# Kernel optimization log

Measured on AMD Instinct MI355X. Metric: run time of the kernel, lower is better.

The kernel has to match this reference:

```python
import jax, jax.numpy as jnp
import numpy as np

HIDDEN = 512
NHEADS = 8
ALPHA = 0.1
NUM_HOP = 4
MASK_VAL = -16384.0
LN_EPS = 1e-5


def setup_inputs() -> dict:
    key = jax.random.key(0)
    ks = jax.random.split(key, 10)
    B, N, H = 8, 1024, HIDDEN
    s = 1.0 / np.sqrt(H)
    x = jax.random.normal(ks[0], (B, N, H), dtype=jnp.float32)
    adj = jax.random.randint(ks[1], (B, N, N), 0, 2, dtype=jnp.int32)
    Wq = jax.random.uniform(ks[2], (H, H), jnp.float32, -s, s)
    bq = jax.random.uniform(ks[3], (H,), jnp.float32, -s, s)
    Wk = jax.random.uniform(ks[4], (H, H), jnp.float32, -s, s)
    bk = jax.random.uniform(ks[5], (H,), jnp.float32, -s, s)
    Wv = jax.random.uniform(ks[6], (H, H), jnp.float32, -s, s)
    bv = jax.random.uniform(ks[7], (H,), jnp.float32, -s, s)
    gamma = jnp.ones((H,), jnp.float32)
    beta = jnp.zeros((H,), jnp.float32)
    return {"x": x, "adj": adj, "Wq": Wq, "bq": bq, "Wk": Wk, "bk": bk,
            "Wv": Wv, "bv": bv, "gamma": gamma, "beta": beta}


def reference(x, adj, Wq, bq, Wk, bk, Wv, bv, gamma, beta):
    B, N, H = x.shape
    u = H // NHEADS
    # torch Linear: y = x @ W^T + b
    q = x @ Wq.T + bq  # [B,N,H]
    k = x @ Wk.T + bk
    v = x @ Wv.T + bv
    # split hidden into contiguous head chunks (matches per-head slicing)
    qh = q.reshape(B, N, NHEADS, u).transpose(0, 2, 1, 3)  # [B,Hd,N,u]
    kh = k.reshape(B, N, NHEADS, u).transpose(0, 2, 1, 3)
    vh = v.reshape(B, N, NHEADS, u).transpose(0, 2, 1, 3)
    scores = jnp.einsum('bhnd,bhmd->bhnm', qh, kh)  # [B,Hd,N,N]
    mask = (adj == 0)[:, None, :, :]  # broadcast over heads
    scores = jnp.where(mask, MASK_VAL, scores)
    pros = jax.nn.softmax(scores, axis=-1)
    z_init = vh
    z = z_init
    for _ in range(NUM_HOP):
        z = (1.0 - ALPHA) * jnp.einsum('bhnm,bhmd->bhnd', pros, z) + ALPHA * z_init
    h_prime = z.transpose(0, 2, 1, 3).reshape(B, N, H)  # concat heads
    y = x + h_prime
    mu = jnp.mean(y, axis=-1, keepdims=True)
    var = jnp.mean((y - mu) ** 2, axis=-1, keepdims=True)
    return (y - mu) / jnp.sqrt(var + LN_EPS) * gamma + beta
```

## Files before the change

### kernel.cpp

```cpp
#include <hip/hip_runtime.h>
#include <hip/hip_bf16.h>

#define BB 8
#define NN 1024
#define HH 512
#define NHEADS 8
#define UU 64

typedef __attribute__((ext_vector_type(8))) short short8;
typedef __attribute__((ext_vector_type(4))) float f32x4;
typedef __attribute__((ext_vector_type(16))) float f32x16;
typedef unsigned short u16;
typedef unsigned char u8;

__device__ inline float b2f(unsigned short u) {
    union { float f; unsigned int i; } c; c.i = ((unsigned int)u) << 16; return c.f;
}
__device__ inline unsigned short f2b(float f) {
    __hip_bfloat16 h = __float2bfloat16(f);
    return *reinterpret_cast<unsigned short*>(&h);
}
__device__ inline unsigned int pkbf(float a, float b) {
    unsigned int r;
    asm("v_cvt_pk_bf16_f32 %0, %1, %2" : "=v"(r) : "v"(a), "v"(b));
    return r;
}
__device__ inline float upk_lo(unsigned int u) {
    union { float f; unsigned int i; } c; c.i = u << 16; return c.f;
}
__device__ inline float upk_hi(unsigned int u) {
    union { float f; unsigned int i; } c; c.i = u & 0xffff0000u; return c.f;
}
__device__ inline void gl_lds16(const void* g, void* l) {
    __builtin_amdgcn_global_load_lds(
        (const __attribute__((address_space(1))) unsigned int*)g,
        (__attribute__((address_space(3))) unsigned int*)l, 16, 0, 0);
}

__global__ __launch_bounds__(256) void cvt_all(
    const float* __restrict__ x, const float* __restrict__ Wq,
    const float* __restrict__ Wk, const float* __restrict__ Wv,
    u16* __restrict__ xb, u16* __restrict__ Wb)
{
    const int gid = blockIdx.x;
    const float* src;
    u16* dst;
    int base;
    if (gid < 2048) {
        src = x; dst = xb;
        base = (gid * 256 + threadIdx.x) * 8;
    } else {
        const int g = gid - 2048;
        const int which = g >> 7;
        const int slice = g & 127;
        src = which == 0 ? Wq : (which == 1 ? Wk : Wv);
        dst = Wb + (size_t)which * HH * HH;
        base = (slice * 256 + threadIdx.x) * 8;
    }
    const float4* sp = (const float4*)&src[base];
    float4 a = sp[0], b = sp[1];
    short8 o;
    o[0] = (short)f2b(a.x); o[1] = (short)f2b(a.y);
    o[2] = (short)f2b(a.z); o[3] = (short)f2b(a.w);
    o[4] = (short)f2b(b.x); o[5] = (short)f2b(b.y);
    o[6] = (short)f2b(b.z); o[7] = (short)f2b(b.w);
    *(short8*)&dst[base] = o;
}

__global__ __launch_bounds__(256) void adj_pack(
    const int* __restrict__ adj, unsigned int* __restrict__ adjpT)
{
    const int wave = threadIdx.x >> 6, lane = threadIdx.x & 63;
    const int row = blockIdx.x * 4 + wave;
    const int b = row >> 10, r = row & 1023;
    const int* ar = adj + (size_t)row * NN;
    unsigned int* ob = adjpT + (((size_t)b) << 15) + r;
    #pragma unroll
    for (int it = 0; it < 16; ++it) {
        int a = ar[it * 64 + lane];
        unsigned long long m = __ballot(a != 0);
        if (lane == 0) {
            ob[(size_t)(2 * it)     << 10] = (unsigned int)m;
            ob[(size_t)(2 * it + 1) << 10] = (unsigned int)(m >> 32);
        }
    }
}

__global__ __launch_bounds__(256, 4) void qkv_gemm(
    const u16* __restrict__ xb, const u16* __restrict__ Wb,
    const float* __restrict__ bq, const float* __restrict__ bk,
    const float* __restrict__ bv,
    u16* __restrict__ q, u16* __restrict__ k, u16* __restrict__ v)
{
    const int which = blockIdx.z;
    const u16* W      = Wb + (size_t)which * HH * HH;
    const float* bias = which == 0 ? bq : (which == 1 ? bk : bv);
    u16* out          = which == 0 ? q  : (which == 1 ? k  : v);

    const int tid = threadIdx.x;
    const int wave = tid >> 6, lane = tid & 63;
    const int ln = lane & 15, quad = lane >> 4;
    const int wr = (wave >> 1) * 64, wc = (wave & 1) * 64;
    const int rowbase = blockIdx.x * 128, colbase = blockIdx.y * 128;

    __shared__ __align__(16) char smem[128 * 136 * 2];
    u16* Cs = (u16*)smem;

    f32x4 acc[4][4];
    #pragma unroll
    for (int ri = 0; ri < 4; ++ri)
        #pragma unroll
        for (int ci = 0; ci < 4; ++ci) acc[ri][ci] = (f32x4){0.f, 0.f, 0.f, 0.f};

    const int lr = lane >> 2;
    const int sg = lane & 3;

    auto STAGE = [&](int buf, int kk) {
        char* Ab = smem + buf * 16384;
        char* Bb = smem + 8192 + buf * 16384;
        #pragma unroll
        for (int i = 0; i < 2; ++i) {
            int r = wave * 32 + i * 16 + lr;
            gl_lds16(&xb[(size_t)(rowbase + r) * HH + kk + sg * 8],
                     Ab + (wave * 32 + i * 16) * 64);
            gl_lds16(&W[(size_t)(colbase + r) * HH + kk + sg * 8],
                     Bb + (wave * 32 + i * 16) * 64);
        }
    };

    STAGE(0, 0);
    for (int s = 0; s < 16; ++s) {
        __syncthreads();
        if (s < 15) STAGE((s + 1) & 1, (s + 1) * 32);
        const u16* As = (const u16*)(smem + (s & 1) * 16384);
        const u16* Bs = (const u16*)(smem + 8192 + (s & 1) * 16384);

        short8 bfr[4];
        #pragma unroll
        for (int ci = 0; ci < 4; ++ci)
            bfr[ci] = *(const short8*)&Bs[(wc + ci * 16 + ln) * 32 + quad * 8];
        #pragma unroll
        for (int ri = 0; ri < 4; ++ri) {
            short8 af = *(const short8*)&As[(wr + ri * 16 + ln) * 32 + quad * 8];
            #pragma unroll
            for (int ci = 0; ci < 4; ++ci)
                acc[ri][ci] = __builtin_amdgcn_mfma_f32_16x16x32_bf16(af, bfr[ci], acc[ri][ci], 0, 0, 0);
        }
    }

    __syncthreads();
    #pragma unroll
    for (int ci = 0; ci < 4; ++ci) {
        int col = wc + ci * 16 + ln;
        float bb = bias[colbase + col];
        #pragma unroll
        for (int ri = 0; ri < 4; ++ri) {
            #pragma unroll
            for (int r = 0; r < 4; ++r) {
                int row = wr + ri * 16 + quad * 4 + r;
                Cs[row * 136 + col] = f2b(acc[ri][ci][r] + bb);
            }
        }
    }
    __syncthreads();
    {
        int row = tid >> 1, half = tid & 1;
        int gcol0 = colbase + half * 64;
        int hh = gcol0 >> 6;
        int grow = rowbase + row;
        int bidx = grow >> 10, n = grow & 1023;
        u16* op = &out[(((size_t)(bidx * NHEADS + hh)) * NN + n) * UU];
        const u16* cp = &Cs[row * 136 + half * 64];
        #pragma unroll
        for (int j = 0; j < 8; ++j)
            *(short8*)(op + j * 8) = *(const short8*)(cp + j * 8);
    }
}

__global__ __launch_bounds__(256) void vt8(
    const u16* __restrict__ v, u8* __restrict__ v8t)
{
    const int bh = blockIdx.x >> 4, chunk = blockIdx.x & 15;
    const int t = threadIdx.x;
    const size_t hd = (size_t)bh << 16;
    __shared__ u16 tile[64][72];

    const int n0 = chunk * 64;
    const int r = t >> 2, cs = t & 3;
    const u16* vp = &v[((size_t)bh * NN + n0 + r) * UU + cs * 16];
    short8 a = *(const short8*)vp;
    short8 b8 = *(const short8*)(vp + 8);
    #pragma unroll
    for (int j = 0; j < 8; ++j) {
        tile[r][cs * 16 + j] = (u16)a[j];
        tile[r][cs * 16 + 8 + j] = (u16)b8[j];
    }
    __syncthreads();
    const int c = t & 63, qt = t >> 6;
    unsigned int w[4];
    #pragma unroll
    for (int g = 0; g < 4; ++g) {
        float f0 = b2f(tile[qt * 16 + g * 4 + 0][c]);
        float f1 = b2f(tile[qt * 16 + g * 4 + 1][c]);
        float f2 = b2f(tile[qt * 16 + g * 4 + 2][c]);
        float f3 = b2f(tile[qt * 16 + g * 4 + 3][c]);
        int lo = __builtin_amdgcn_cvt_pk_fp8_f32(f0, f1, 0, false);
        w[g] = (unsigned int)__builtin_amdgcn_cvt_pk_fp8_f32(f2, f3, lo, true);
    }
    uint4 o; o.x = w[0]; o.y = w[1]; o.z = w[2]; o.w = w[3];
    *(uint4*)&v8t[hd + (size_t)c * 1024 + n0 + qt * 16] = o;
}

__device__ inline f32x16 score_tile(const u16* kp, const short8* qf)
{
    short8 kf[4];
    #pragma unroll
    for (int f = 0; f < 4; ++f) kf[f] = *(const short8*)(kp + f * 16);
    f32x16 acc;
    #pragma unroll
    for (int j = 0; j < 16; ++j) acc[j] = 0.f;
    #pragma unroll
    for (int f = 0; f < 4; ++f)
        acc = __builtin_amdgcn_mfma_f32_32x32x16_bf16(kf[f], qf[f], acc, 0, 0, 0);
    return acc;
}

__global__ __launch_bounds__(512, 4) void scores_softmax(
    const u16* __restrict__ q, const u16* __restrict__ kmat,
    const unsigned int* __restrict__ adjpT, u8* __restrict__ P8)
{
    const int gid = blockIdx.x;
    const int j = gid >> 3;
    const int h = gid & 7;
    const int b = j >> 5;
    const int bx = j & 31;
    const int bh = b * NHEADS + h;

    const int tid = threadIdx.x;
    const int kq = tid >> 6, lane = tid & 63;
    const int l31 = lane & 31, hi = lane >> 5;
    const int n = bx * 32 + l31;
    const int kt0 = kq * 4;

    __shared__ float rs[8][32];

    short8 qf[4];
    const u16* qp = &q[((size_t)bh * NN + n) * UU + hi * 8];
    #pragma unroll
    for (int f = 0; f < 4; ++f) qf[f] = *(const short8*)(qp + f * 16);

    const u16* kbase = kmat + (size_t)bh * NN * UU + (size_t)(kt0 * 32 + l31) * UU + hi * 8;
    const unsigned int* mbase = adjpT + (((size_t)b) << 15) + n;

    unsigned int mv[4];
    #pragma unroll
    for (int i = 0; i < 4; ++i)
        mv[i] = mbase[(size_t)(kt0 + i) << 10] >> (4 * hi);

    const float L2E = 1.442695041f;
    const float C0 = -46.16624f;
    const float CM = -100000.0f;

    unsigned int eb[4][4][2];
    float rs0 = 0.f, rs1 = 0.f, rs2 = 0.f, rs3 = 0.f;
    #pragma unroll
    for (int i = 0; i < 4; ++i) {
        f32x16 acc = score_tile(kbase + (size_t)i * (32 * UU), qf);
        const unsigned int m2 = mv[i];
        #pragma unroll
        for (int g = 0; g < 4; ++g) {
            float e[4];
            #pragma unroll
            for (int r = 0; r < 4; ++r) {
                const int koff = r + 8 * g;
                float addv = ((m2 >> koff) & 1u) ? C0 : CM;
                e[r] = __builtin_amdgcn_exp2f(fmaf(L2E, acc[g * 4 + r], addv));
            }
            if (g == 0) rs0 += (e[0] + e[1]) + (e[2] + e[3]);
            else if (g == 1) rs1 += (e[0] + e[1]) + (e[2] + e[3]);
            else if (g == 2) rs2 += (e[0] + e[1]) + (e[2] + e[3]);
            else rs3 += (e[0] + e[1]) + (e[2] + e[3]);
            eb[i][g][0] = pkbf(e[0], e[1]);
            eb[i][g][1] = pkbf(e[2], e[3]);
        }
    }
    float rsum = (rs0 + rs1) + (rs2 + rs3);
    rsum += __shfl_xor(rsum, 32);
    if (lane < 32) rs[kq][lane] = rsum;
    __syncthreads();
    const float total = ((rs[0][l31] + rs[1][l31]) + (rs[2][l31] + rs[3][l31]))
                      + ((rs[4][l31] + rs[5][l31]) + (rs[6][l31] + rs[7][l31]));
    const float scl = 16.0f / total;

    u8* pb = P8 + (((size_t)bh) << 20) + (size_t)(n >> 4) * 16384
           + (n & 15) * 32 + hi * 16;
    #pragma unroll
    for (int i = 0; i < 4; ++i) {
        unsigned int dw[4];
        #pragma unroll
        for (int g = 0; g < 4; ++g) {
            float e0 = upk_lo(eb[i][g][0]) * scl;
            float e1 = upk_hi(eb[i][g][0]) * scl;
            float e2 = upk_lo(eb[i][g][1]) * scl;
            float e3 = upk_hi(eb[i][g][1]) * scl;
            int lo = __builtin_amdgcn_cvt_pk_fp8_f32(e0, e1, 0, false);
            dw[g] = (unsigned int)__builtin_amdgcn_cvt_pk_fp8_f32(e2, e3, lo, true);
        }
        unsigned int sendA = hi ? dw[0] : dw[2];
        unsigned int sendB = hi ? dw[1] : dw[3];
        unsigned int recvA = (unsigned int)__shfl_xor((int)sendA, 32);
        unsigned int recvB = (unsigned int)__shfl_xor((int)sendB, 32);
        uint4 o;
        o.x = hi ? recvA : dw[0];
        o.y = hi ? dw[2] : recvA;
        o.z = hi ? recvB : dw[1];
        o.w = hi ? dw[3] : recvB;
        *(uint4*)(pb + (size_t)(kt0 + i) * 512) = o;
    }
}

__global__ __launch_bounds__(512) void hop(
    const u8* __restrict__ P8, const u8* __restrict__ z8in,
    const u16* __restrict__ v, u8* __restrict__ z8out,
    u16* __restrict__ zbf_out, int last)
{
    const int b = blockIdx.z, h = blockIdx.y, rt = blockIdx.x;
    const int bh = b * NHEADS + h;
    const int tid = threadIdx.x;
    const int wave = tid >> 6, lane = tid & 63;
    const int ln = lane & 15, quad = lane >> 4;
    const int wrow = rt * 128 + wave * 16;

    __shared__ __align__(16) u8 zt[64 * 1040];

    const u8* zg = z8in + ((size_t)bh << 16);
    #pragma unroll
    for (int i = 0; i < 8; ++i) {
        int c = wave * 8 + i;
        gl_lds16(zg + (size_t)c * 1024 + lane * 16, (char*)zt + c * 1040);
    }

    const u8* pt = P8 + ((size_t)bh << 20) + (size_t)(rt * 8 + wave) * 16384
                 + ln * 32 + quad * 8;
    long pa[4];
    #pragma unroll
    for (int i = 0; i < 4; ++i) pa[i] = *(const long*)(pt + i * 512);

    __syncthreads();

    f32x4 acc[4];
    #pragma unroll
    for (int ci = 0; ci < 4; ++ci) acc[ci] = (f32x4){0.f, 0.f, 0.f, 0.f};

    #pragma unroll
    for (int kc = 0; kc < 32; ++kc) {
        long a = pa[kc & 3];
        if (kc + 4 < 32) pa[kc & 3] = *(const long*)(pt + (kc + 4) * 512);
        int kk = kc * 32;
        #pragma unroll
        for (int ci = 0; ci < 4; ++ci) {
            long bz = *(const long*)&zt[(ci * 16 + ln) * 1040 + kk + quad * 8];
            acc[ci] = __builtin_amdgcn_mfma_f32_16x16x32_fp8_fp8(a, bz, acc[ci], 0, 0, 0);
        }
    }

    if (last) {
        #pragma unroll
        for (int ci = 0; ci < 4; ++ci) {
            int col = ci * 16 + ln;
            #pragma unroll
            for (int r = 0; r < 4; ++r) {
                int row = wrow + quad * 4 + r;
                float vv = b2f(v[((size_t)bh * NN + row) * UU + col]);
                zbf_out[((size_t)(b * NN + row)) * HH + h * UU + col]
                    = f2b(0.05625f * acc[ci][r] + 0.1f * vv);
            }
        }
    } else {
        u8* zo = z8out + ((size_t)bh << 16);
        #pragma unroll
        for (int ci = 0; ci < 4; ++ci) {
            int col = ci * 16 + ln;
            float zv[4];
            #pragma unroll
            for (int r = 0; r < 4; ++r) {
                int row = wrow + quad * 4 + r;
                float vv = b2f(v[((size_t)bh * NN + row) * UU + col]);
                zv[r] = 0.05625f * acc[ci][r] + 0.1f * vv;
            }
            int lo = __builtin_amdgcn_cvt_pk_fp8_f32(zv[0], zv[1], 0, false);
            unsigned int dw = (unsigned int)__builtin_amdgcn_cvt_pk_fp8_f32(zv[2], zv[3], lo, true);
            *(unsigned int*)&zo[(size_t)col * 1024 + wrow + quad * 4] = dw;
        }
    }
}

__global__ __launch_bounds__(256) void resid_ln(
    const float* __restrict__ x, const u16* __restrict__ z,
    const float* __restrict__ gamma, const float* __restrict__ beta,
    float* __restrict__ out)
{
    const int r = blockIdx.x * 4 + (threadIdx.x >> 6);
    const int lane = threadIdx.x & 63;
    const size_t base = (size_t)r * HH + lane * 8;

    const float4* xp = (const float4*)&x[base];
    float4 x0 = xp[0], x1 = xp[1];
    short8 zv = *(const short8*)&z[base];
    float y[8];
    y[0] = x0.x + b2f((u16)zv[0]); y[1] = x0.y + b2f((u16)zv[1]);
    y[2] = x0.z + b2f((u16)zv[2]); y[3] = x0.w + b2f((u16)zv[3]);
    y[4] = x1.x + b2f((u16)zv[4]); y[5] = x1.y + b2f((u16)zv[5]);
    y[6] = x1.z + b2f((u16)zv[6]); y[7] = x1.w + b2f((u16)zv[7]);

    float s = 0.f, sq = 0.f;
    #pragma unroll
    for (int j = 0; j < 8; ++j) { s += y[j]; sq += y[j] * y[j]; }
    #pragma unroll
    for (int off = 32; off >= 1; off >>= 1) {
        s  += __shfl_xor(s, off);
        sq += __shfl_xor(sq, off);
    }
    const float mu = s * (1.0f / HH);
    const float var = sq * (1.0f / HH) - mu * mu;
    const float rstd = rsqrtf(var + 1e-5f);

    const float4* gp = (const float4*)&gamma[lane * 8];
    const float4* bp = (const float4*)&beta[lane * 8];
    float4 g0 = gp[0], g1 = gp[1], b0 = bp[0], b1 = bp[1];

    float4 o0, o1;
    o0.x = (y[0] - mu) * rstd * g0.x + b0.x;
    o0.y = (y[1] - mu) * rstd * g0.y + b0.y;
    o0.z = (y[2] - mu) * rstd * g0.z + b0.z;
    o0.w = (y[3] - mu) * rstd * g0.w + b0.w;
    o1.x = (y[4] - mu) * rstd * g1.x + b1.x;
    o1.y = (y[5] - mu) * rstd * g1.y + b1.y;
    o1.z = (y[6] - mu) * rstd * g1.z + b1.z;
    o1.w = (y[7] - mu) * rstd * g1.w + b1.w;
    float4* op = (float4*)&out[base];
    op[0] = o0; op[1] = o1;
}

extern "C" void kernel_launch(void* const* d_in, const int* in_sizes, int n_in,
                              void* d_out, int out_size, void* d_ws, size_t ws_size,
                              hipStream_t stream)
{
    const float* x   = (const float*)d_in[0];
    const int* adj   = (const int*)d_in[1];
    const float* Wq  = (const float*)d_in[2];
    const float* bq  = (const float*)d_in[3];
    const float* Wk  = (const float*)d_in[4];
    const float* bk  = (const float*)d_in[5];
    const float* Wv  = (const float*)d_in[6];
    const float* bv  = (const float*)d_in[7];
    const float* gamma = (const float*)d_in[8];
    const float* beta  = (const float*)d_in[9];
    float* out = (float*)d_out;

    const size_t E = (size_t)BB * NN * HH;
    u16* ws16 = (u16*)d_ws;
    u16* xb = ws16;
    u16* q  = ws16 + E;
    u16* k  = ws16 + 2 * E;
    u16* v  = ws16 + 3 * E;
    u16* za = ws16 + 4 * E;
    u16* Wb = ws16 + 5 * E;
    u8* base8 = (u8*)(ws16 + 5 * E + 786432);
    u8* P8  = base8;
    u8* z8a = base8 + ((size_t)64 << 20);
    u8* z8b = z8a + ((size_t)4 << 20);
    u8* v8t = z8b + ((size_t)4 << 20);
    unsigned int* adjpT = (unsigned int*)(v8t + ((size_t)4 << 20));

    cvt_all<<<dim3(2432), 256, 0, stream>>>(x, Wq, Wk, Wv, xb, Wb);
    adj_pack<<<dim3(2048), 256, 0, stream>>>(adj, adjpT);
    qkv_gemm<<<dim3(64, 4, 3), 256, 0, stream>>>(xb, Wb, bq, bk, bv, q, k, v);
    vt8<<<dim3(1024), 256, 0, stream>>>(v, v8t);
    scores_softmax<<<dim3(2048), 512, 0, stream>>>(q, k, adjpT, P8);
    hop<<<dim3(8, NHEADS, BB), 512, 0, stream>>>(P8, v8t, v, z8a, za, 0);
    hop<<<dim3(8, NHEADS, BB), 512, 0, stream>>>(P8, z8a, v, z8b, za, 0);
    hop<<<dim3(8, NHEADS, BB), 512, 0, stream>>>(P8, z8b, v, z8a, za, 0);
    hop<<<dim3(8, NHEADS, BB), 512, 0, stream>>>(P8, z8a, v, z8b, za, 1);
    resid_ln<<<dim3(2048), 256, 0, stream>>>(x, za, gamma, beta, out);
}
```

Measured before the change: 265.0 us.

## Fuse prep kernels and load hop z operand directly from global

Merges the bf16 conversion and adjacency bit-packing kernels into one launch, saving one kernel launch. The hop kernel no longer stages z into LDS with a block barrier. It instead double-buffers z fragments in registers from global/L2. Its grid is flattened to 1D with head as the fastest index and launch bounds raised for occupancy. This trades LDS reuse across waves for redundant global reads of z, relying on L2 to serve them.

```diff
diff --git a/kernel.cpp b/kernel.cpp
--- a/kernel.cpp
+++ b/kernel.cpp
@@ -37,51 +37,51 @@
         (__attribute__((address_space(3))) unsigned int*)l, 16, 0, 0);
 }
 
-__global__ __launch_bounds__(256) void cvt_all(
+__global__ __launch_bounds__(256) void prep(
     const float* __restrict__ x, const float* __restrict__ Wq,
     const float* __restrict__ Wk, const float* __restrict__ Wv,
-    u16* __restrict__ xb, u16* __restrict__ Wb)
+    const int* __restrict__ adj,
+    u16* __restrict__ xb, u16* __restrict__ Wb,
+    unsigned int* __restrict__ adjpT)
 {
     const int gid = blockIdx.x;
-    const float* src;
-    u16* dst;
-    int base;
-    if (gid < 2048) {
-        src = x; dst = xb;
-        base = (gid * 256 + threadIdx.x) * 8;
+    if (gid < 2432) {
+        const float* src;
+        u16* dst;
+        int base;
+        if (gid < 2048) {
+            src = x; dst = xb;
+            base = (gid * 256 + threadIdx.x) * 8;
+        } else {
+            const int g = gid - 2048;
+            const int which = g >> 7;
+            const int slice = g & 127;
+            src = which == 0 ? Wq : (which == 1 ? Wk : Wv);
+            dst = Wb + (size_t)which * HH * HH;
+            base = (slice * 256 + threadIdx.x) * 8;
+        }
+        const float4* sp = (const float4*)&src[base];
+        float4 a = sp[0], b = sp[1];
+        short8 o;
+        o[0] = (short)f2b(a.x); o[1] = (short)f2b(a.y);
+        o[2] = (short)f2b(a.z); o[3] = (short)f2b(a.w);
+        o[4] = (short)f2b(b.x); o[5] = (short)f2b(b.y);
+        o[6] = (short)f2b(b.z); o[7] = (short)f2b(b.w);
+        *(short8*)&dst[base] = o;
     } else {
-        const int g = gid - 2048;
-        const int which = g >> 7;
-        const int slice = g & 127;
-        src = which == 0 ? Wq : (which == 1 ? Wk : Wv);
-        dst = Wb + (size_t)which * HH * HH;
-        base = (slice * 256 + threadIdx.x) * 8;
-    }
-    const float4* sp = (const float4*)&src[base];
-    float4 a = sp[0], b = sp[1];
-    short8 o;
-    o[0] = (short)f2b(a.x); o[1] = (short)f2b(a.y);
-    o[2] = (short)f2b(a.z); o[3] = (short)f2b(a.w);
-    o[4] = (short)f2b(b.x); o[5] = (short)f2b(b.y);
-    o[6] = (short)f2b(b.z); o[7] = (short)f2b(b.w);
-    *(short8*)&dst[base] = o;
-}
-
-__global__ __launch_bounds__(256) void adj_pack(
-    const int* __restrict__ adj, unsigned int* __restrict__ adjpT)
-{
-    const int wave = threadIdx.x >> 6, lane = threadIdx.x & 63;
-    const int row = blockIdx.x * 4 + wave;
-    const int b = row >> 10, r = row & 1023;
-    const int* ar = adj + (size_t)row * NN;
-    unsigned int* ob = adjpT + (((size_t)b) << 15) + r;
-    #pragma unroll
-    for (int it = 0; it < 16; ++it) {
-        int a = ar[it * 64 + lane];
-        unsigned long long m = __ballot(a != 0);
-        if (lane == 0) {
-            ob[(size_t)(2 * it)     << 10] = (unsigned int)m;
-            ob[(size_t)(2 * it + 1) << 10] = (unsigned int)(m >> 32);
+        const int wave = threadIdx.x >> 6, lane = threadIdx.x & 63;
+        const int row = (gid - 2432) * 4 + wave;
+        const int b = row >> 10, r = row & 1023;
+        const int* ar = adj + (size_t)row * NN;
+        unsigned int* ob = adjpT + (((size_t)b) << 15) + r;
+        #pragma unroll
+        for (int it = 0; it < 16; ++it) {
+            int a = ar[it * 64 + lane];
+            unsigned long long m = __ballot(a != 0);
+            if (lane == 0) {
+                ob[(size_t)(2 * it)     << 10] = (unsigned int)m;
+                ob[(size_t)(2 * it + 1) << 10] = (unsigned int)(m >> 32);
+            }
         }
     }
 }
@@ -319,34 +319,35 @@
     }
 }
 
-__global__ __launch_bounds__(512) void hop(
+__global__ __launch_bounds__(512, 4) void hop(
     const u8* __restrict__ P8, const u8* __restrict__ z8in,
     const u16* __restrict__ v, u8* __restrict__ z8out,
     u16* __restrict__ zbf_out, int last)
 {
-    const int b = blockIdx.z, h = blockIdx.y, rt = blockIdx.x;
+    const int gid = blockIdx.x;
+    const int h = gid & 7;
+    const int j = gid >> 3;
+    const int b = j >> 3;
+    const int rt = j & 7;
     const int bh = b * NHEADS + h;
+
     const int tid = threadIdx.x;
     const int wave = tid >> 6, lane = tid & 63;
     const int ln = lane & 15, quad = lane >> 4;
     const int wrow = rt * 128 + wave * 16;
 
-    __shared__ __align__(16) u8 zt[64 * 1040];
-
-    const u8* zg = z8in + ((size_t)bh << 16);
-    #pragma unroll
-    for (int i = 0; i < 8; ++i) {
-        int c = wave * 8 + i;
-        gl_lds16(zg + (size_t)c * 1024 + lane * 16, (char*)zt + c * 1040);
-    }
-
+    const u8* zg = z8in + ((size_t)bh << 16) + (size_t)ln * 1024 + quad * 8;
     const u8* pt = P8 + ((size_t)bh << 20) + (size_t)(rt * 8 + wave) * 16384
                  + ln * 32 + quad * 8;
+
     long pa[4];
     #pragma unroll
     for (int i = 0; i < 4; ++i) pa[i] = *(const long*)(pt + i * 512);
 
-    __syncthreads();
+    long zb0[4], zb1[4];
+    #pragma unroll
+    for (int ci = 0; ci < 4; ++ci)
+        zb0[ci] = *(const long*)(zg + (size_t)ci * 16384);
 
     f32x4 acc[4];
     #pragma unroll
@@ -354,12 +355,23 @@
 
     #pragma unroll
     for (int kc = 0; kc < 32; ++kc) {
+        if (kc + 1 < 32) {
+            const int kk = (kc + 1) * 32;
+            if (kc & 1) {
+                #pragma unroll
+                for (int ci = 0; ci < 4; ++ci)
+                    zb0[ci] = *(const long*)(zg + (size_t)ci * 16384 + kk);
+            } else {
+                #pragma unroll
+                for (int ci = 0; ci < 4; ++ci)
+                    zb1[ci] = *(const long*)(zg + (size_t)ci * 16384 + kk);
+            }
+        }
         long a = pa[kc & 3];
         if (kc + 4 < 32) pa[kc & 3] = *(const long*)(pt + (kc + 4) * 512);
-        int kk = kc * 32;
         #pragma unroll
         for (int ci = 0; ci < 4; ++ci) {
-            long bz = *(const long*)&zt[(ci * 16 + ln) * 1040 + kk + quad * 8];
+            long bz = (kc & 1) ? zb1[ci] : zb0[ci];
             acc[ci] = __builtin_amdgcn_mfma_f32_16x16x32_fp8_fp8(a, bz, acc[ci], 0, 0, 0);
         }
     }
@@ -473,14 +485,13 @@
     u8* v8t = z8b + ((size_t)4 << 20);
     unsigned int* adjpT = (unsigned int*)(v8t + ((size_t)4 << 20));
 
-    cvt_all<<<dim3(2432), 256, 0, stream>>>(x, Wq, Wk, Wv, xb, Wb);
-    adj_pack<<<dim3(2048), 256, 0, stream>>>(adj, adjpT);
+    prep<<<dim3(4480), 256, 0, stream>>>(x, Wq, Wk, Wv, adj, xb, Wb, adjpT);
     qkv_gemm<<<dim3(64, 4, 3), 256, 0, stream>>>(xb, Wb, bq, bk, bv, q, k, v);
     vt8<<<dim3(1024), 256, 0, stream>>>(v, v8t);
     scores_softmax<<<dim3(2048), 512, 0, stream>>>(q, k, adjpT, P8);
-    hop<<<dim3(8, NHEADS, BB), 512, 0, stream>>>(P8, v8t, v, z8a, za, 0);
-    hop<<<dim3(8, NHEADS, BB), 512, 0, stream>>>(P8, z8a, v, z8b, za, 0);
-    hop<<<dim3(8, NHEADS, BB), 512, 0, stream>>>(P8, z8b, v, z8a, za, 0);
-    hop<<<dim3(8, NHEADS, BB), 512, 0, stream>>>(P8, z8a, v, z8b, za, 1);
+    hop<<<dim3(512), 512, 0, stream>>>(P8, v8t, v, z8a, za, 0);
+    hop<<<dim3(512), 512, 0, stream>>>(P8, z8a, v, z8b, za, 0);
+    hop<<<dim3(512), 512, 0, stream>>>(P8, z8b, v, z8a, za, 0);
+    hop<<<dim3(512), 512, 0, stream>>>(P8, z8a, v, z8b, za, 1);
     resid_ln<<<dim3(2048), 256, 0, stream>>>(x, za, gamma, beta, out);
 }
```

Result: slower. 443.4 us (+67.3%).

## Merge conversion and adjacency-packing kernels; halve hop LDS with two-phase staging

Applied to the files above, without the earlier changes.

The bf16 conversion and adjacency bit-packing kernels are merged into one launch so that one kernel boundary goes away. The hop kernel now stages the z tile into LDS in two 512-column halves, which halves its shared-memory footprint. It also declares launch bounds of four blocks per CU, aiming for higher occupancy. The cost is an extra pair of barriers mid-loop, and the second half's staging is not overlapped with compute. The row-pair interleaved LDS layout also changes the bank access pattern.

```diff
diff --git a/kernel.cpp b/kernel.cpp
--- a/kernel.cpp
+++ b/kernel.cpp
@@ -37,51 +37,51 @@
         (__attribute__((address_space(3))) unsigned int*)l, 16, 0, 0);
 }
 
-__global__ __launch_bounds__(256) void cvt_all(
+__global__ __launch_bounds__(256) void prep(
     const float* __restrict__ x, const float* __restrict__ Wq,
     const float* __restrict__ Wk, const float* __restrict__ Wv,
-    u16* __restrict__ xb, u16* __restrict__ Wb)
+    const int* __restrict__ adj,
+    u16* __restrict__ xb, u16* __restrict__ Wb,
+    unsigned int* __restrict__ adjpT)
 {
     const int gid = blockIdx.x;
-    const float* src;
-    u16* dst;
-    int base;
-    if (gid < 2048) {
-        src = x; dst = xb;
-        base = (gid * 256 + threadIdx.x) * 8;
+    if (gid < 2432) {
+        const float* src;
+        u16* dst;
+        int base;
+        if (gid < 2048) {
+            src = x; dst = xb;
+            base = (gid * 256 + threadIdx.x) * 8;
+        } else {
+            const int g = gid - 2048;
+            const int which = g >> 7;
+            const int slice = g & 127;
+            src = which == 0 ? Wq : (which == 1 ? Wk : Wv);
+            dst = Wb + (size_t)which * HH * HH;
+            base = (slice * 256 + threadIdx.x) * 8;
+        }
+        const float4* sp = (const float4*)&src[base];
+        float4 a = sp[0], b = sp[1];
+        short8 o;
+        o[0] = (short)f2b(a.x); o[1] = (short)f2b(a.y);
+        o[2] = (short)f2b(a.z); o[3] = (short)f2b(a.w);
+        o[4] = (short)f2b(b.x); o[5] = (short)f2b(b.y);
+        o[6] = (short)f2b(b.z); o[7] = (short)f2b(b.w);
+        *(short8*)&dst[base] = o;
     } else {
-        const int g = gid - 2048;
-        const int which = g >> 7;
-        const int slice = g & 127;
-        src = which == 0 ? Wq : (which == 1 ? Wk : Wv);
-        dst = Wb + (size_t)which * HH * HH;
-        base = (slice * 256 + threadIdx.x) * 8;
-    }
-    const float4* sp = (const float4*)&src[base];
-    float4 a = sp[0], b = sp[1];
-    short8 o;
-    o[0] = (short)f2b(a.x); o[1] = (short)f2b(a.y);
-    o[2] = (short)f2b(a.z); o[3] = (short)f2b(a.w);
-    o[4] = (short)f2b(b.x); o[5] = (short)f2b(b.y);
-    o[6] = (short)f2b(b.z); o[7] = (short)f2b(b.w);
-    *(short8*)&dst[base] = o;
-}
-
-__global__ __launch_bounds__(256) void adj_pack(
-    const int* __restrict__ adj, unsigned int* __restrict__ adjpT)
-{
-    const int wave = threadIdx.x >> 6, lane = threadIdx.x & 63;
-    const int row = blockIdx.x * 4 + wave;
-    const int b = row >> 10, r = row & 1023;
-    const int* ar = adj + (size_t)row * NN;
-    unsigned int* ob = adjpT + (((size_t)b) << 15) + r;
-    #pragma unroll
-    for (int it = 0; it < 16; ++it) {
-        int a = ar[it * 64 + lane];
-        unsigned long long m = __ballot(a != 0);
-        if (lane == 0) {
-            ob[(size_t)(2 * it)     << 10] = (unsigned int)m;
-            ob[(size_t)(2 * it + 1) << 10] = (unsigned int)(m >> 32);
+        const int wave = threadIdx.x >> 6, lane = threadIdx.x & 63;
+        const int row = (gid - 2432) * 4 + wave;
+        const int b = row >> 10, r = row & 1023;
+        const int* ar = adj + (size_t)row * NN;
+        unsigned int* ob = adjpT + (((size_t)b) << 15) + r;
+        #pragma unroll
+        for (int it = 0; it < 16; ++it) {
+            int a = ar[it * 64 + lane];
+            unsigned long long m = __ballot(a != 0);
+            if (lane == 0) {
+                ob[(size_t)(2 * it)     << 10] = (unsigned int)m;
+                ob[(size_t)(2 * it + 1) << 10] = (unsigned int)(m >> 32);
+            }
         }
     }
 }
@@ -319,7 +319,7 @@
     }
 }
 
-__global__ __launch_bounds__(512) void hop(
+__global__ __launch_bounds__(512, 4) void hop(
     const u8* __restrict__ P8, const u8* __restrict__ z8in,
     const u16* __restrict__ v, u8* __restrict__ z8out,
     u16* __restrict__ zbf_out, int last)
@@ -331,17 +331,23 @@
     const int ln = lane & 15, quad = lane >> 4;
     const int wrow = rt * 128 + wave * 16;
 
-    __shared__ __align__(16) u8 zt[64 * 1040];
+    __shared__ __align__(16) u8 zt[32 * 1040];
 
     const u8* zg = z8in + ((size_t)bh << 16);
-    #pragma unroll
-    for (int i = 0; i < 8; ++i) {
-        int c = wave * 8 + i;
-        gl_lds16(zg + (size_t)c * 1024 + lane * 16, (char*)zt + c * 1040);
-    }
+    auto STAGEZ = [&](int m0) {
+        #pragma unroll
+        for (int jj = 0; jj < 4; ++jj) {
+            int g = jj * 8 + wave;
+            const u8* src = zg + (size_t)(2 * g + (lane >> 5)) * 1024 + m0
+                          + (lane & 31) * 16;
+            gl_lds16(src, (char*)zt + g * 1040);
+        }
+    };
 
     const u8* pt = P8 + ((size_t)bh << 20) + (size_t)(rt * 8 + wave) * 16384
                  + ln * 32 + quad * 8;
+
+    STAGEZ(0);
     long pa[4];
     #pragma unroll
     for (int i = 0; i < 4; ++i) pa[i] = *(const long*)(pt + i * 512);
@@ -353,13 +359,31 @@
     for (int ci = 0; ci < 4; ++ci) acc[ci] = (f32x4){0.f, 0.f, 0.f, 0.f};
 
     #pragma unroll
-    for (int kc = 0; kc < 32; ++kc) {
+    for (int kc = 0; kc < 16; ++kc) {
+        long a = pa[kc & 3];
+        pa[kc & 3] = *(const long*)(pt + (kc + 4) * 512);
+        int kkl = kc * 32;
+        #pragma unroll
+        for (int ci = 0; ci < 4; ++ci) {
+            int row = ci * 16 + ln;
+            long bz = *(const long*)&zt[(row >> 1) * 1040 + (row & 1) * 512 + kkl + quad * 8];
+            acc[ci] = __builtin_amdgcn_mfma_f32_16x16x32_fp8_fp8(a, bz, acc[ci], 0, 0, 0);
+        }
+    }
+
+    __syncthreads();
+    STAGEZ(512);
+    __syncthreads();
+
+    #pragma unroll
+    for (int kc = 16; kc < 32; ++kc) {
         long a = pa[kc & 3];
         if (kc + 4 < 32) pa[kc & 3] = *(const long*)(pt + (kc + 4) * 512);
-        int kk = kc * 32;
+        int kkl = kc * 32 - 512;
         #pragma unroll
         for (int ci = 0; ci < 4; ++ci) {
-            long bz = *(const long*)&zt[(ci * 16 + ln) * 1040 + kk + quad * 8];
+            int row = ci * 16 + ln;
+            long bz = *(const long*)&zt[(row >> 1) * 1040 + (row & 1) * 512 + kkl + quad * 8];
             acc[ci] = __builtin_amdgcn_mfma_f32_16x16x32_fp8_fp8(a, bz, acc[ci], 0, 0, 0);
         }
     }
@@ -473,8 +497,7 @@
     u8* v8t = z8b + ((size_t)4 << 20);
     unsigned int* adjpT = (unsigned int*)(v8t + ((size_t)4 << 20));
 
-    cvt_all<<<dim3(2432), 256, 0, stream>>>(x, Wq, Wk, Wv, xb, Wb);
-    adj_pack<<<dim3(2048), 256, 0, stream>>>(adj, adjpT);
+    prep<<<dim3(4480), 256, 0, stream>>>(x, Wq, Wk, Wv, adj, xb, Wb, adjpT);
     qkv_gemm<<<dim3(64, 4, 3), 256, 0, stream>>>(xb, Wb, bq, bk, bv, q, k, v);
     vt8<<<dim3(1024), 256, 0, stream>>>(v, v8t);
     scores_softmax<<<dim3(2048), 512, 0, stream>>>(q, k, adjpT, P8);
```

After: 269.3 us. About the same (+1.6%).

## Merge prep kernels, fuse V fp8 transpose into QKV GEMM, prefetch K tiles

Applied to the files above, without the earlier changes.

Merges the x/W bf16 conversion and the adjacency bit-packing into one launch. The V transpose-to-fp8 pass moves into the QKV GEMM epilogue, which reads the bf16 tile already in shared memory instead of re-reading v from global memory. This removes two kernel launches and one pass over V. The scores kernel now loads the next K tile's fragments before the softmax math of the current tile, so global loads overlap compute at the cost of extra registers.

```diff
diff --git a/kernel.cpp b/kernel.cpp
--- a/kernel.cpp
+++ b/kernel.cpp
@@ -37,51 +37,51 @@
         (__attribute__((address_space(3))) unsigned int*)l, 16, 0, 0);
 }
 
-__global__ __launch_bounds__(256) void cvt_all(
+__global__ __launch_bounds__(256) void prep(
     const float* __restrict__ x, const float* __restrict__ Wq,
     const float* __restrict__ Wk, const float* __restrict__ Wv,
-    u16* __restrict__ xb, u16* __restrict__ Wb)
+    const int* __restrict__ adj,
+    u16* __restrict__ xb, u16* __restrict__ Wb,
+    unsigned int* __restrict__ adjpT)
 {
     const int gid = blockIdx.x;
-    const float* src;
-    u16* dst;
-    int base;
-    if (gid < 2048) {
-        src = x; dst = xb;
-        base = (gid * 256 + threadIdx.x) * 8;
+    if (gid < 2432) {
+        const float* src;
+        u16* dst;
+        int base;
+        if (gid < 2048) {
+            src = x; dst = xb;
+            base = (gid * 256 + threadIdx.x) * 8;
+        } else {
+            const int g = gid - 2048;
+            const int which = g >> 7;
+            const int slice = g & 127;
+            src = which == 0 ? Wq : (which == 1 ? Wk : Wv);
+            dst = Wb + (size_t)which * HH * HH;
+            base = (slice * 256 + threadIdx.x) * 8;
+        }
+        const float4* sp = (const float4*)&src[base];
+        float4 a = sp[0], b = sp[1];
+        short8 o;
+        o[0] = (short)f2b(a.x); o[1] = (short)f2b(a.y);
+        o[2] = (short)f2b(a.z); o[3] = (short)f2b(a.w);
+        o[4] = (short)f2b(b.x); o[5] = (short)f2b(b.y);
+        o[6] = (short)f2b(b.z); o[7] = (short)f2b(b.w);
+        *(short8*)&dst[base] = o;
     } else {
-        const int g = gid - 2048;
-        const int which = g >> 7;
-        const int slice = g & 127;
-        src = which == 0 ? Wq : (which == 1 ? Wk : Wv);
-        dst = Wb + (size_t)which * HH * HH;
-        base = (slice * 256 + threadIdx.x) * 8;
-    }
-    const float4* sp = (const float4*)&src[base];
-    float4 a = sp[0], b = sp[1];
-    short8 o;
-    o[0] = (short)f2b(a.x); o[1] = (short)f2b(a.y);
-    o[2] = (short)f2b(a.z); o[3] = (short)f2b(a.w);
-    o[4] = (short)f2b(b.x); o[5] = (short)f2b(b.y);
-    o[6] = (short)f2b(b.z); o[7] = (short)f2b(b.w);
-    *(short8*)&dst[base] = o;
-}
-
-__global__ __launch_bounds__(256) void adj_pack(
-    const int* __restrict__ adj, unsigned int* __restrict__ adjpT)
-{
-    const int wave = threadIdx.x >> 6, lane = threadIdx.x & 63;
-    const int row = blockIdx.x * 4 + wave;
-    const int b = row >> 10, r = row & 1023;
-    const int* ar = adj + (size_t)row * NN;
-    unsigned int* ob = adjpT + (((size_t)b) << 15) + r;
-    #pragma unroll
-    for (int it = 0; it < 16; ++it) {
-        int a = ar[it * 64 + lane];
-        unsigned long long m = __ballot(a != 0);
-        if (lane == 0) {
-            ob[(size_t)(2 * it)     << 10] = (unsigned int)m;
-            ob[(size_t)(2 * it + 1) << 10] = (unsigned int)(m >> 32);
+        const int wave = threadIdx.x >> 6, lane = threadIdx.x & 63;
+        const int row = (gid - 2432) * 4 + wave;
+        const int b = row >> 10, r = row & 1023;
+        const int* ar = adj + (size_t)row * NN;
+        unsigned int* ob = adjpT + (((size_t)b) << 15) + r;
+        #pragma unroll
+        for (int it = 0; it < 16; ++it) {
+            int a = ar[it * 64 + lane];
+            unsigned long long m = __ballot(a != 0);
+            if (lane == 0) {
+                ob[(size_t)(2 * it)     << 10] = (unsigned int)m;
+                ob[(size_t)(2 * it + 1) << 10] = (unsigned int)(m >> 32);
+            }
         }
     }
 }
@@ -90,7 +90,8 @@
     const u16* __restrict__ xb, const u16* __restrict__ Wb,
     const float* __restrict__ bq, const float* __restrict__ bk,
     const float* __restrict__ bv,
-    u16* __restrict__ q, u16* __restrict__ k, u16* __restrict__ v)
+    u16* __restrict__ q, u16* __restrict__ k, u16* __restrict__ v,
+    u8* __restrict__ v8t)
 {
     const int which = blockIdx.z;
     const u16* W      = Wb + (size_t)which * HH * HH;
@@ -175,54 +176,24 @@
         for (int j = 0; j < 8; ++j)
             *(short8*)(op + j * 8) = *(const short8*)(cp + j * 8);
     }
-}
-
-__global__ __launch_bounds__(256) void vt8(
-    const u16* __restrict__ v, u8* __restrict__ v8t)
-{
-    const int bh = blockIdx.x >> 4, chunk = blockIdx.x & 15;
-    const int t = threadIdx.x;
-    const size_t hd = (size_t)bh << 16;
-    __shared__ u16 tile[64][72];
-
-    const int n0 = chunk * 64;
-    const int r = t >> 2, cs = t & 3;
-    const u16* vp = &v[((size_t)bh * NN + n0 + r) * UU + cs * 16];
-    short8 a = *(const short8*)vp;
-    short8 b8 = *(const short8*)(vp + 8);
-    #pragma unroll
-    for (int j = 0; j < 8; ++j) {
-        tile[r][cs * 16 + j] = (u16)a[j];
-        tile[r][cs * 16 + 8 + j] = (u16)b8[j];
-    }
-    __syncthreads();
-    const int c = t & 63, qt = t >> 6;
-    unsigned int w[4];
-    #pragma unroll
-    for (int g = 0; g < 4; ++g) {
-        float f0 = b2f(tile[qt * 16 + g * 4 + 0][c]);
-        float f1 = b2f(tile[qt * 16 + g * 4 + 1][c]);
-        float f2 = b2f(tile[qt * 16 + g * 4 + 2][c]);
-        float f3 = b2f(tile[qt * 16 + g * 4 + 3][c]);
-        int lo = __builtin_amdgcn_cvt_pk_fp8_f32(f0, f1, 0, false);
-        w[g] = (unsigned int)__builtin_amdgcn_cvt_pk_fp8_f32(f2, f3, lo, true);
-    }
-    uint4 o; o.x = w[0]; o.y = w[1]; o.z = w[2]; o.w = w[3];
-    *(uint4*)&v8t[hd + (size_t)c * 1024 + n0 + qt * 16] = o;
-}
-
-__device__ inline f32x16 score_tile(const u16* kp, const short8* qf)
-{
-    short8 kf[4];
-    #pragma unroll
-    for (int f = 0; f < 4; ++f) kf[f] = *(const short8*)(kp + f * 16);
-    f32x16 acc;
-    #pragma unroll
-    for (int j = 0; j < 16; ++j) acc[j] = 0.f;
-    #pragma unroll
-    for (int f = 0; f < 4; ++f)
-        acc = __builtin_amdgcn_mfma_f32_32x32x16_bf16(kf[f], qf[f], acc, 0, 0, 0);
-    return acc;
+    if (which == 2) {
+        const int d_local = tid >> 1, nh = tid & 1;
+        const int hloc = d_local >> 6, d = d_local & 63;
+        const int bidx = rowbase >> 10, n0 = (rowbase & 1023) + nh * 64;
+        const int bh = bidx * NHEADS + (colbase >> 6) + hloc;
+        u8* vp = v8t + ((size_t)bh << 16) + (size_t)d * 1024 + n0;
+        #pragma unroll
+        for (int j = 0; j < 16; ++j) {
+            const u16* cp = &Cs[(nh * 64 + j * 4) * 136 + d_local];
+            float f0 = b2f(cp[0]);
+            float f1 = b2f(cp[136]);
+            float f2 = b2f(cp[272]);
+            float f3 = b2f(cp[408]);
+            int lo = __builtin_amdgcn_cvt_pk_fp8_f32(f0, f1, 0, false);
+            unsigned int dw = (unsigned int)__builtin_amdgcn_cvt_pk_fp8_f32(f2, f3, lo, true);
+            *(unsigned int*)(vp + j * 4) = dw;
+        }
+    }
 }
 
 __global__ __launch_bounds__(512, 4) void scores_softmax(
@@ -263,9 +234,24 @@
 
     unsigned int eb[4][4][2];
     float rs0 = 0.f, rs1 = 0.f, rs2 = 0.f, rs3 = 0.f;
+
+    short8 kf[4];
+    #pragma unroll
+    for (int f = 0; f < 4; ++f) kf[f] = *(const short8*)(kbase + f * 16);
+
     #pragma unroll
     for (int i = 0; i < 4; ++i) {
-        f32x16 acc = score_tile(kbase + (size_t)i * (32 * UU), qf);
+        f32x16 acc;
+        #pragma unroll
+        for (int jj = 0; jj < 16; ++jj) acc[jj] = 0.f;
+        #pragma unroll
+        for (int f = 0; f < 4; ++f)
+            acc = __builtin_amdgcn_mfma_f32_32x32x16_bf16(kf[f], qf[f], acc, 0, 0, 0);
+        if (i < 3) {
+            const u16* kn = kbase + (size_t)(i + 1) * (32 * UU);
+            #pragma unroll
+            for (int f = 0; f < 4; ++f) kf[f] = *(const short8*)(kn + f * 16);
+        }
         const unsigned int m2 = mv[i];
         #pragma unroll
         for (int g = 0; g < 4; ++g) {
@@ -473,10 +459,8 @@
     u8* v8t = z8b + ((size_t)4 << 20);
     unsigned int* adjpT = (unsigned int*)(v8t + ((size_t)4 << 20));
 
-    cvt_all<<<dim3(2432), 256, 0, stream>>>(x, Wq, Wk, Wv, xb, Wb);
-    adj_pack<<<dim3(2048), 256, 0, stream>>>(adj, adjpT);
-    qkv_gemm<<<dim3(64, 4, 3), 256, 0, stream>>>(xb, Wb, bq, bk, bv, q, k, v);
-    vt8<<<dim3(1024), 256, 0, stream>>>(v, v8t);
+    prep<<<dim3(4480), 256, 0, stream>>>(x, Wq, Wk, Wv, adj, xb, Wb, adjpT);
+    qkv_gemm<<<dim3(64, 4, 3), 256, 0, stream>>>(xb, Wb, bq, bk, bv, q, k, v, v8t);
     scores_softmax<<<dim3(2048), 512, 0, stream>>>(q, k, adjpT, P8);
     hop<<<dim3(8, NHEADS, BB), 512, 0, stream>>>(P8, v8t, v, z8a, za, 0);
     hop<<<dim3(8, NHEADS, BB), 512, 0, stream>>>(P8, z8a, v, z8b, za, 0);
```

Result: no change. 261.8 us (median of 2 runs) (-1.2%).
